# Kernel tuning notes

Hardware: AMD Instinct MI355X
Metric: run time of the kernel (lower is better)

## Reference

```python
import jax, jax.numpy as jnp
import numpy as np

B, S, D, H, DFF = 2, 2048, 1024, 16, 4096
HD = D // H
EPS = 1e-5


def setup_inputs() -> dict:
    key = jax.random.key(0)
    ks = jax.random.split(key, 8)
    s = lambda fan_in: 1.0 / np.sqrt(fan_in)
    return {
        "x": jax.random.normal(ks[0], (B, S, D), jnp.float32),
        "ln1_g": jnp.ones((D,), jnp.float32),
        "ln1_b": jnp.zeros((D,), jnp.float32),
        "Wq": jax.random.normal(ks[1], (D, D), jnp.float32) * s(D),
        "Wk": jax.random.normal(ks[2], (D, D), jnp.float32) * s(D),
        "Wv": jax.random.normal(ks[3], (D, D), jnp.float32) * s(D),
        "Wo": jax.random.normal(ks[4], (D, D), jnp.float32) * s(D),
        "bo": jnp.zeros((D,), jnp.float32),
        "ln2_g": jnp.ones((D,), jnp.float32),
        "ln2_b": jnp.zeros((D,), jnp.float32),
        "W1": jax.random.normal(ks[5], (D, DFF), jnp.float32) * s(D),
        "b1": jnp.zeros((DFF,), jnp.float32),
        "W2": jax.random.normal(ks[6], (DFF, D), jnp.float32) * s(DFF),
        "b2": jnp.zeros((D,), jnp.float32),
    }


def _layernorm(x, g, b):
    mu = jnp.mean(x, axis=-1, keepdims=True)
    var = jnp.var(x, axis=-1, keepdims=True)
    return (x - mu) * jax.lax.rsqrt(var + EPS) * g + b


def reference(x, ln1_g, ln1_b, Wq, Wk, Wv, Wo, bo, ln2_g, ln2_b, W1, b1, W2, b2):
    # --- pre-LN + causal multi-head attention + residual ---
    h = _layernorm(x, ln1_g, ln1_b)
    q = (h @ Wq).reshape(B, S, H, HD).transpose(0, 2, 1, 3)  # [B,H,S,hd]
    k = (h @ Wk).reshape(B, S, H, HD).transpose(0, 2, 1, 3)
    v = (h @ Wv).reshape(B, S, H, HD).transpose(0, 2, 1, 3)
    scores = jnp.einsum("bhqd,bhkd->bhqk", q, k) / jnp.sqrt(jnp.float32(HD))
    causal = jnp.triu(jnp.ones((S, S), bool), k=1)  # True above diagonal -> masked
    scores = jnp.where(causal, -jnp.inf, scores)
    attn = jax.nn.softmax(scores, axis=-1)  # dropout is identity at inference
    ctx = jnp.einsum("bhqk,bhkd->bhqd", attn, v)
    ctx = ctx.transpose(0, 2, 1, 3).reshape(B, S, D)
    x = x + ctx @ Wo + bo
    # --- pre-LN + MLP + residual ---
    h = _layernorm(x, ln2_g, ln2_b)
    h = jax.nn.gelu(h @ W1 + b1, approximate=False)  # torch nn.GELU default = exact
    x = x + h @ W2 + b2
    return x
```

## Files before the change

kernel.cpp:

```cpp
#include <hip/hip_runtime.h>
#include <hip/hip_bf16.h>
#include <math.h>

using bf16 = __hip_bfloat16;
typedef short bf16x8 __attribute__((ext_vector_type(8)));
typedef float f32x4 __attribute__((ext_vector_type(4)));

static constexpr int B = 2, S = 2048, D = 1024, H = 16, HD = 64, DFF = 4096;
static constexpr int NR = B * S;
static constexpr int DQ = 3072;
static constexpr float EPS = 1e-5f;

__device__ __forceinline__ bf16 f2b(float v) { return __float2bfloat16(v); }

typedef __attribute__((address_space(1))) const void* gp1_t;
typedef __attribute__((address_space(3))) void* sp3_t;
__device__ __forceinline__ void gld_lds16(const bf16* g, bf16* l) {
    __builtin_amdgcn_global_load_lds((gp1_t)(const void*)g, (sp3_t)(void*)l, 16, 0, 0);
}

__device__ __forceinline__ void convT_body(const float* __restrict__ src,
                                           bf16* __restrict__ dst,
                                           int K, int N, int k0, int n0, int tid) {
    __shared__ float tile[64][65];
    const int r = tid >> 4, c = (tid & 15) * 4;
#pragma unroll
    for (int rr = 0; rr < 64; rr += 16) {
        float4 v = *(const float4*)&src[(size_t)(k0 + r + rr) * N + n0 + c];
        tile[r + rr][c] = v.x; tile[r + rr][c + 1] = v.y;
        tile[r + rr][c + 2] = v.z; tile[r + rr][c + 3] = v.w;
    }
    __syncthreads();
    const int n = tid >> 2, ks = (tid & 3) * 16;
    union { bf16 h[16]; int4 v2[2]; } o;
#pragma unroll
    for (int i = 0; i < 16; ++i) o.h[i] = f2b(tile[ks + i][n]);
    bf16* dp = &dst[(size_t)(n0 + n) * K + k0 + ks];
    *(int4*)dp = o.v2[0];
    *(int4*)(dp + 8) = o.v2[1];
}

__global__ __launch_bounds__(256) void convT_kernel(const float* __restrict__ src,
                                                    bf16* __restrict__ dst,
                                                    int K, int N) {
    convT_body(src, dst, K, N, blockIdx.x * 64, blockIdx.y * 64, threadIdx.x);
}

__global__ __launch_bounds__(256) void convT5_kernel(const float* __restrict__ Wq,
                                                     const float* __restrict__ Wk,
                                                     const float* __restrict__ Wv,
                                                     const float* __restrict__ Wo,
                                                     const float* __restrict__ W2,
                                                     bf16* __restrict__ WqkvT,
                                                     bf16* __restrict__ WoT,
                                                     bf16* __restrict__ W2T) {
    const int bid = blockIdx.x;
    const float* src;
    bf16* dst;
    int K, N, bx, by;
    if (bid < 768) {
        const int j = bid >> 8, r = bid & 255;
        src = (j == 0) ? Wq : ((j == 1) ? Wk : Wv);
        dst = WqkvT + (size_t)j * D * D;
        K = D; N = D; bx = r & 15; by = r >> 4;
    } else if (bid < 1024) {
        const int r = bid - 768;
        src = Wo; dst = WoT; K = D; N = D; bx = r & 15; by = r >> 4;
    } else {
        const int r = bid - 1024;
        src = W2; dst = W2T; K = DFF; N = D; bx = r & 63; by = r >> 6;
    }
    convT_body(src, dst, K, N, bx * 64, by * 64, threadIdx.x);
}

__global__ __launch_bounds__(256) void ln_kernel(const float* __restrict__ x,
                                                 const float* __restrict__ g,
                                                 const float* __restrict__ b,
                                                 bf16* __restrict__ out) {
    const int row = blockIdx.x;
    const int tid = threadIdx.x;
    const float4 v4 = ((const float4*)(x + (size_t)row * D))[tid];
    float v[4] = {v4.x, v4.y, v4.z, v4.w};
    float s = v[0] + v[1] + v[2] + v[3];
    float sq = v[0] * v[0] + v[1] * v[1] + v[2] * v[2] + v[3] * v[3];
#pragma unroll
    for (int off = 32; off >= 1; off >>= 1) {
        s += __shfl_xor(s, off);
        sq += __shfl_xor(sq, off);
    }
    __shared__ float ssum[4], ssq[4];
    const int wave = tid >> 6;
    if ((tid & 63) == 0) { ssum[wave] = s; ssq[wave] = sq; }
    __syncthreads();
    s = ssum[0] + ssum[1] + ssum[2] + ssum[3];
    sq = ssq[0] + ssq[1] + ssq[2] + ssq[3];
    const float mu = s * (1.0f / D);
    const float var = sq * (1.0f / D) - mu * mu;
    const float rstd = rsqrtf(var + EPS);
    bf16* orow = out + (size_t)row * D;
#pragma unroll
    for (int i = 0; i < 4; ++i) {
        const int c = tid * 4 + i;
        orow[c] = f2b((v[i] - mu) * rstd * g[c] + b[c]);
    }
}

template <int EPI, int BN, int TPB>
__global__ __launch_bounds__(256) void gemm_bt(const bf16* __restrict__ A,
                                               const bf16* __restrict__ Bt,
                                               const float* __restrict__ bias,
                                               const float* __restrict__ res,
                                               void* __restrict__ Cv,
                                               int M, int N, int K) {
    constexpr int NTW = BN / 32;
    constexpr int AHALF = 128 * 32;
    constexpr int BHALF = BN * 32;
    constexpr int ASZ = 2 * AHALF, BSZ = 2 * BHALF;
    constexpr int CST = BN + 8;
    __shared__ __align__(16) bf16 smem[2 * (ASZ + BSZ)];

    const int Mtiles = M / 128;
    const int p = blockIdx.x;
    const int tm = p % Mtiles;
    const int tn0 = (p / Mtiles) * TPB;
    const int tid = threadIdx.x;
    const int wave = tid >> 6, lane = tid & 63;
    const int wm = wave >> 1, wn = wave & 1;
    const int quad = lane >> 4, l16 = lane & 15;

    const int r4 = tid >> 2, s4 = (tid & 3) * 8;
    const size_t K64 = (size_t)64 * K;
    const int nk = K / 64;

    for (int tp = 0; tp < TPB; ++tp) {
        const int tn = tn0 + tp;
        if (tp) __syncthreads();

        f32x4 acc[4][NTW];
#pragma unroll
        for (int i = 0; i < 4; ++i)
#pragma unroll
            for (int j = 0; j < NTW; ++j) acc[i][j] = (f32x4){0.f, 0.f, 0.f, 0.f};

        const bf16* Ap = A + (size_t)(tm * 128 + r4) * K + s4;
        const bf16* Bp = Bt + (size_t)(tn * BN + r4) * K + s4;

        gld_lds16(Ap, smem + tid * 8);
        gld_lds16(Ap + K64, smem + (256 + tid) * 8);
        gld_lds16(Ap + 32, smem + (512 + tid) * 8);
        gld_lds16(Ap + K64 + 32, smem + (768 + tid) * 8);
        gld_lds16(Bp, smem + 2 * ASZ + tid * 8);
        gld_lds16(Bp + 32, smem + 2 * ASZ + (256 + tid) * 8);
        Ap += 64;
        Bp += 64;

        for (int kt = 0; kt < nk; ++kt) {
            const int cur = kt & 1, nxt = cur ^ 1;
            bf16* Acur = smem + cur * ASZ;
            bf16* Bcur = smem + 2 * ASZ + cur * BSZ;
            __syncthreads();
            if (kt + 1 < nk) {
                bf16* Anxt = smem + nxt * ASZ;
                bf16* Bnxt = smem + 2 * ASZ + nxt * BSZ;
                gld_lds16(Ap, Anxt + tid * 8);
                gld_lds16(Ap + K64, Anxt + (256 + tid) * 8);
                gld_lds16(Ap + 32, Anxt + (512 + tid) * 8);
                gld_lds16(Ap + K64 + 32, Anxt + (768 + tid) * 8);
                gld_lds16(Bp, Bnxt + tid * 8);
                gld_lds16(Bp + 32, Bnxt + (256 + tid) * 8);
                Ap += 64;
                Bp += 64;
            }

#pragma unroll
            for (int ks = 0; ks < 2; ++ks) {
                const bf16* Ah = Acur + ks * AHALF;
                const bf16* Bh = Bcur + ks * BHALF;
                bf16x8 aF[4], bF[NTW];
#pragma unroll
                for (int mt = 0; mt < 4; ++mt)
                    aF[mt] = *(const bf16x8*)(Ah + (wm * 64 + mt * 16 + l16) * 32 + quad * 8);
#pragma unroll
                for (int nt = 0; nt < NTW; ++nt)
                    bF[nt] = *(const bf16x8*)(Bh + (wn * (BN / 2) + nt * 16 + l16) * 32 + quad * 8);
#pragma unroll
                for (int mt = 0; mt < 4; ++mt)
#pragma unroll
                    for (int nt = 0; nt < NTW; ++nt)
                        acc[mt][nt] = __builtin_amdgcn_mfma_f32_16x16x32_bf16(
                            aF[mt], bF[nt], acc[mt][nt], 0, 0, 0);
            }
        }

        if constexpr (EPI == 1) {
#pragma unroll
            for (int nt = 0; nt < NTW; ++nt) {
                const int col = tn * BN + wn * (BN / 2) + nt * 16 + l16;
                const float bv = bias[col];
#pragma unroll
                for (int mt = 0; mt < 4; ++mt) {
                    const int row0 = tm * 128 + wm * 64 + mt * 16 + quad * 4;
#pragma unroll
                    for (int j = 0; j < 4; ++j) {
                        const size_t idx = (size_t)(row0 + j) * N + col;
                        ((float*)Cv)[idx] = acc[mt][nt][j] + bv + res[idx];
                    }
                }
            }
        } else {
            bf16* C = (bf16*)Cv;
            __syncthreads();
#pragma unroll
            for (int nt = 0; nt < NTW; ++nt) {
                const int ccol = wn * (BN / 2) + nt * 16 + l16;
                float bv = 0.f;
                if (EPI == 2) bv = bias[tn * BN + ccol];
#pragma unroll
                for (int mt = 0; mt < 4; ++mt) {
                    const int r0 = wm * 64 + mt * 16 + quad * 4;
#pragma unroll
                    for (int j = 0; j < 4; ++j) {
                        float v = acc[mt][nt][j];
                        if (EPI == 2) {
                            v += bv;
                            v = 0.5f * v * (1.0f + erff(v * 0.70710678118654752f));
                        }
                        smem[(r0 + j) * CST + ccol] = f2b(v);
                    }
                }
            }
            __syncthreads();
            bf16* crow = C + (size_t)(tm * 128) * N + tn * BN;
#pragma unroll
            for (int i = 0; i < BN / 16; ++i) {
                const int gid = i * 256 + tid;
                const int row = gid / (BN / 8), c8 = gid % (BN / 8);
                const int4 val = *(const int4*)(smem + row * CST + c8 * 8);
                *(int4*)(crow + (size_t)row * N + c8 * 8) = val;
            }
        }
    }
}

__global__ __launch_bounds__(256) void fattn_kernel(const bf16* __restrict__ QKV,
                                                    bf16* __restrict__ ctx) {
    const int id = blockIdx.x;
    const int bh = id & 31;
    const int k = id >> 5;
    const int t = (k < 16) ? 31 - k : k - 16;
    const int b = bh >> 4, h = bh & (H - 1);
    const int tid = threadIdx.x;
    const int wave = tid >> 6, lane = tid & 63;
    const int quad = lane >> 4, l16 = lane & 15;
    const bf16* Qp = QKV + (size_t)b * S * DQ + h * HD;
    const bf16* Kp = Qp + D;
    const bf16* Vp = Qp + 2 * D;

    __shared__ __align__(16) bf16 Ks[2][64 * 64];
    __shared__ __align__(16) bf16 Vt[2][64][72];

    const int keyA = tid >> 3;
    const int sA = (keyA & 3) | ((keyA >> 1) & 4);
    const int dsA = ((tid & 7) ^ sA) * 8;
    const size_t K32 = (size_t)32 * DQ;

    const int q0 = t * 64;
    const bf16* qg = Qp + (size_t)(q0 + wave * 16 + l16) * DQ + quad * 8;
    union U8 { bf16 h[8]; bf16x8 v; };
    U8 uq0, uq1;
    uq0.v = *(const bf16x8*)(qg);
    uq1.v = *(const bf16x8*)(qg + 32);
#pragma unroll
    for (int i = 0; i < 8; ++i) {
        uq0.h[i] = f2b(__bfloat162float(uq0.h[i]) * 0.125f);
        uq1.h[i] = f2b(__bfloat162float(uq1.h[i]) * 0.125f);
    }
    const bf16x8 aQ0 = uq0.v;
    const bf16x8 aQ1 = uq1.v;

    const int kb = (l16 >> 2) * 8 + (l16 & 3);
    const int sQ = (l16 & 3) | (((l16 >> 2) & 1) << 2);
    const int ofs0 = kb * 64 + ((quad ^ sQ) * 8);
    const int ofs1 = kb * 64 + (((4 + quad) ^ sQ) * 8);

    f32x4 O[4];
#pragma unroll
    for (int nt = 0; nt < 4; ++nt) O[nt] = (f32x4){0.f, 0.f, 0.f, 0.f};
    float rowm = -3.0e38f, rowl = 0.f;

    gld_lds16(Kp + (size_t)keyA * DQ + dsA, Ks[0] + tid * 8);
    gld_lds16(Kp + K32 + (size_t)keyA * DQ + dsA, Ks[0] + (256 + tid) * 8);
    {
        const bf16* vg = Vp + (size_t)lane * DQ + wave * 16;
        U8 u0, u1;
        u0.v = *(const bf16x8*)vg;
        u1.v = *(const bf16x8*)(vg + 8);
#pragma unroll
        for (int i = 0; i < 8; ++i) {
            Vt[0][wave * 16 + i][lane] = u0.h[i];
            Vt[0][wave * 16 + 8 + i][lane] = u1.h[i];
        }
    }

    const int nch = t + 1;
    for (int c = 0; c < nch; ++c) {
        const int cur = c & 1, nxt = cur ^ 1;
        __syncthreads();
        U8 u0, u1;
        if (c + 1 < nch) {
            const bf16* kg = Kp + (size_t)((c + 1) * 64 + keyA) * DQ + dsA;
            gld_lds16(kg, Ks[nxt] + tid * 8);
            gld_lds16(kg + K32, Ks[nxt] + (256 + tid) * 8);
            const bf16* vg = Vp + (size_t)((c + 1) * 64 + lane) * DQ + wave * 16;
            u0.v = *(const bf16x8*)vg;
            u1.v = *(const bf16x8*)(vg + 8);
        }

        f32x4 sc[4];
        __builtin_amdgcn_s_setprio(1);
#pragma unroll
        for (int m = 0; m < 4; ++m) {
            const bf16* kr = Ks[cur] + (m & 1) * 256 + (m >> 1) * 2048;
            const bf16x8 bK0 = *(const bf16x8*)(kr + ofs0);
            const bf16x8 bK1 = *(const bf16x8*)(kr + ofs1);
            f32x4 z = (f32x4){0.f, 0.f, 0.f, 0.f};
            z = __builtin_amdgcn_mfma_f32_16x16x32_bf16(bK0, aQ0, z, 0, 0, 0);
            z = __builtin_amdgcn_mfma_f32_16x16x32_bf16(bK1, aQ1, z, 0, 0, 0);
            sc[m] = z;
        }
        __builtin_amdgcn_s_setprio(0);
        if (c == nch - 1) {
            const int qloc = wave * 16 + l16;
#pragma unroll
            for (int m = 0; m < 4; ++m) {
                const int kk = quad * 8 + (m & 1) * 4 + (m >> 1) * 32;
#pragma unroll
                for (int j = 0; j < 4; ++j)
                    if (kk + j > qloc) sc[m][j] = -3.0e38f;
            }
        }
        f32x4 mv;
#pragma unroll
        for (int j = 0; j < 4; ++j)
            mv[j] = fmaxf(fmaxf(sc[0][j], sc[1][j]), fmaxf(sc[2][j], sc[3][j]));
        float mx = fmaxf(fmaxf(mv[0], mv[1]), fmaxf(mv[2], mv[3]));
        mx = fmaxf(mx, __shfl_xor(mx, 16));
        mx = fmaxf(mx, __shfl_xor(mx, 32));
        const float mn = fmaxf(rowm, mx);
        const float alq = __expf(rowm - mn);
        rowm = mn;
        float rs = 0.f;
#pragma unroll
        for (int m = 0; m < 4; ++m)
#pragma unroll
            for (int j = 0; j < 4; ++j) {
                sc[m][j] = __expf(sc[m][j] - mn);
                rs += sc[m][j];
            }
        rs += __shfl_xor(rs, 16);
        rs += __shfl_xor(rs, 32);
        rowl = rowl * alq + rs;

        U8 p0, p1;
#pragma unroll
        for (int j = 0; j < 4; ++j) {
            p0.h[j]     = f2b(sc[0][j]);
            p0.h[4 + j] = f2b(sc[1][j]);
            p1.h[j]     = f2b(sc[2][j]);
            p1.h[4 + j] = f2b(sc[3][j]);
        }
#pragma unroll
        for (int nt = 0; nt < 4; ++nt)
#pragma unroll
            for (int j = 0; j < 4; ++j) O[nt][j] *= alq;
        __builtin_amdgcn_s_setprio(1);
#pragma unroll
        for (int nt = 0; nt < 4; ++nt) {
            const bf16x8 bV0 = *(const bf16x8*)&Vt[cur][nt * 16 + l16][quad * 8];
            const bf16x8 bV1 = *(const bf16x8*)&Vt[cur][nt * 16 + l16][32 + quad * 8];
            O[nt] = __builtin_amdgcn_mfma_f32_16x16x32_bf16(bV0, p0.v, O[nt], 0, 0, 0);
            O[nt] = __builtin_amdgcn_mfma_f32_16x16x32_bf16(bV1, p1.v, O[nt], 0, 0, 0);
        }
        __builtin_amdgcn_s_setprio(0);
        if (c + 1 < nch) {
#pragma unroll
            for (int i = 0; i < 8; ++i) {
                Vt[nxt][wave * 16 + i][lane] = u0.h[i];
                Vt[nxt][wave * 16 + 8 + i][lane] = u1.h[i];
            }
        }
    }

    const float rlq = 1.0f / rowl;
    bf16* crow = ctx + (size_t)b * S * D + h * HD + (size_t)(q0 + wave * 16 + l16) * D;
#pragma unroll
    for (int nt = 0; nt < 4; ++nt) {
        union { bf16 h[4]; int2 v; } o;
#pragma unroll
        for (int j = 0; j < 4; ++j) o.h[j] = f2b(O[nt][j] * rlq);
        *(int2*)(crow + nt * 16 + quad * 4) = o.v;
    }
}

extern "C" void kernel_launch(void* const* d_in, const int* in_sizes, int n_in,
                              void* d_out, int out_size, void* d_ws, size_t ws_size,
                              hipStream_t stream) {
    const float* x     = (const float*)d_in[0];
    const float* ln1_g = (const float*)d_in[1];
    const float* ln1_b = (const float*)d_in[2];
    const float* Wq    = (const float*)d_in[3];
    const float* Wk    = (const float*)d_in[4];
    const float* Wv    = (const float*)d_in[5];
    const float* Wo    = (const float*)d_in[6];
    const float* bo    = (const float*)d_in[7];
    const float* ln2_g = (const float*)d_in[8];
    const float* ln2_b = (const float*)d_in[9];
    const float* W1    = (const float*)d_in[10];
    const float* b1    = (const float*)d_in[11];
    const float* W2    = (const float*)d_in[12];
    const float* b2    = (const float*)d_in[13];
    float* out = (float*)d_out;

    char* ws = (char*)d_ws;
    const size_t MB = (size_t)1 << 20;
    bf16* h     = (bf16*)(ws + 0 * MB);
    bf16* W1T   = (bf16*)(ws + 0 * MB);
    bf16* QKVb  = (bf16*)(ws + 8 * MB);
    bf16* hff   = (bf16*)(ws + 8 * MB);
    bf16* ctx   = (bf16*)(ws + 32 * MB);
    bf16* h2    = (bf16*)(ws + 40 * MB);
    bf16* WqkvT = (bf16*)(ws + 48 * MB);
    bf16* WoT   = (bf16*)(ws + 54 * MB);
    bf16* W2T   = (bf16*)(ws + 56 * MB);

    convT5_kernel<<<2048, 256, 0, stream>>>(Wq, Wk, Wv, Wo, W2, WqkvT, WoT, W2T);
    ln_kernel<<<NR, 256, 0, stream>>>(x, ln1_g, ln1_b, h);
    gemm_bt<0, 64, 1><<<(NR / 128) * (DQ / 64), 256, 0, stream>>>(
        h, WqkvT, nullptr, nullptr, QKVb, NR, DQ, D);
    convT_kernel<<<dim3(16, 64), 256, 0, stream>>>(W1, W1T, D, DFF);
    fattn_kernel<<<dim3((S / 64) * B * H), 256, 0, stream>>>(QKVb, ctx);
    gemm_bt<1, 64, 1><<<(NR / 128) * (D / 64), 256, 0, stream>>>(
        ctx, WoT, bo, x, out, NR, D, D);
    ln_kernel<<<NR, 256, 0, stream>>>(out, ln2_g, ln2_b, h2);
    gemm_bt<2, 64, 1><<<(NR / 128) * (DFF / 64), 256, 0, stream>>>(
        h2, W1T, b1, nullptr, hff, NR, DFF, D);
    gemm_bt<1, 64, 1><<<(NR / 128) * (D / 64), 256, 0, stream>>>(
        hff, W2T, b2, out, out, NR, D, DFF);
}
```

Baseline: 334.4 us.

## Use polynomial erf GELU, lazy softmax rescaling, and fuse W1 transpose into batch conversion

Replaces the library erff in the MLP GELU epilogue with an Abramowitz-Stegun rational polynomial using a fast reciprocal and exp. In flash attention, the running max and output rescale are updated only when any lane's chunk max exceeds the current max by more than 8, skipping per-chunk O multiplies. When the workspace is large enough, the W1 transpose is folded into the batched weight-conversion kernel, removing a separate launch. Risks are a small loss of GELU accuracy and larger unnormalized exponentials in attention.

```diff
diff --git a/kernel.cpp b/kernel.cpp
--- a/kernel.cpp
+++ b/kernel.cpp
@@ -12,6 +12,20 @@
 static constexpr float EPS = 1e-5f;
 
 __device__ __forceinline__ bf16 f2b(float v) { return __float2bfloat16(v); }
+
+__device__ __forceinline__ float gelu_exact(float v) {
+    const float u = v * 0.70710678118654752f;
+    const float au = fabsf(u);
+    const float t = __builtin_amdgcn_rcpf(1.0f + 0.3275911f * au);
+    float poly = 1.061405429f;
+    poly = poly * t - 1.453152027f;
+    poly = poly * t + 1.421413741f;
+    poly = poly * t - 0.284496736f;
+    poly = poly * t + 0.254829592f;
+    poly = poly * t;
+    const float ea = 1.0f - poly * __expf(-u * u);
+    return 0.5f * v * (1.0f + copysignf(ea, u));
+}
 
 typedef __attribute__((address_space(1))) const void* gp1_t;
 typedef __attribute__((address_space(3))) void* sp3_t;
@@ -46,14 +60,16 @@
     convT_body(src, dst, K, N, blockIdx.x * 64, blockIdx.y * 64, threadIdx.x);
 }
 
-__global__ __launch_bounds__(256) void convT5_kernel(const float* __restrict__ Wq,
+__global__ __launch_bounds__(256) void convT6_kernel(const float* __restrict__ Wq,
                                                      const float* __restrict__ Wk,
                                                      const float* __restrict__ Wv,
                                                      const float* __restrict__ Wo,
                                                      const float* __restrict__ W2,
+                                                     const float* __restrict__ W1,
                                                      bf16* __restrict__ WqkvT,
                                                      bf16* __restrict__ WoT,
-                                                     bf16* __restrict__ W2T) {
+                                                     bf16* __restrict__ W2T,
+                                                     bf16* __restrict__ W1T) {
     const int bid = blockIdx.x;
     const float* src;
     bf16* dst;
@@ -66,9 +82,12 @@
     } else if (bid < 1024) {
         const int r = bid - 768;
         src = Wo; dst = WoT; K = D; N = D; bx = r & 15; by = r >> 4;
-    } else {
+    } else if (bid < 2048) {
         const int r = bid - 1024;
         src = W2; dst = W2T; K = DFF; N = D; bx = r & 63; by = r >> 6;
+    } else {
+        const int r = bid - 2048;
+        src = W1; dst = W1T; K = D; N = DFF; bx = r & 15; by = r >> 4;
     }
     convT_body(src, dst, K, N, bx * 64, by * 64, threadIdx.x);
 }
@@ -221,10 +240,7 @@
 #pragma unroll
                     for (int j = 0; j < 4; ++j) {
                         float v = acc[mt][nt][j];
-                        if (EPI == 2) {
-                            v += bv;
-                            v = 0.5f * v * (1.0f + erff(v * 0.70710678118654752f));
-                        }
+                        if (EPI == 2) v = gelu_exact(v + bv);
                         smem[(r0 + j) * CST + ccol] = f2b(v);
                     }
                 }
@@ -346,20 +362,27 @@
         float mx = fmaxf(fmaxf(mv[0], mv[1]), fmaxf(mv[2], mv[3]));
         mx = fmaxf(mx, __shfl_xor(mx, 16));
         mx = fmaxf(mx, __shfl_xor(mx, 32));
-        const float mn = fmaxf(rowm, mx);
-        const float alq = __expf(rowm - mn);
-        rowm = mn;
+        if (__any(mx > rowm + 8.0f)) {
+            const float mn = fmaxf(rowm, mx);
+            const float alq = __expf(rowm - mn);
+            rowm = mn;
+            rowl *= alq;
+#pragma unroll
+            for (int nt = 0; nt < 4; ++nt)
+#pragma unroll
+                for (int j = 0; j < 4; ++j) O[nt][j] *= alq;
+        }
         float rs = 0.f;
 #pragma unroll
         for (int m = 0; m < 4; ++m)
 #pragma unroll
             for (int j = 0; j < 4; ++j) {
-                sc[m][j] = __expf(sc[m][j] - mn);
+                sc[m][j] = __expf(sc[m][j] - rowm);
                 rs += sc[m][j];
             }
         rs += __shfl_xor(rs, 16);
         rs += __shfl_xor(rs, 32);
-        rowl = rowl * alq + rs;
+        rowl += rs;
 
         U8 p0, p1;
 #pragma unroll
@@ -369,10 +392,6 @@
             p1.h[j]     = f2b(sc[2][j]);
             p1.h[4 + j] = f2b(sc[3][j]);
         }
-#pragma unroll
-        for (int nt = 0; nt < 4; ++nt)
-#pragma unroll
-            for (int j = 0; j < 4; ++j) O[nt][j] *= alq;
         __builtin_amdgcn_s_setprio(1);
 #pragma unroll
         for (int nt = 0; nt < 4; ++nt) {
@@ -423,8 +442,8 @@
 
     char* ws = (char*)d_ws;
     const size_t MB = (size_t)1 << 20;
+    const bool wide = ws_size >= 72 * MB;
     bf16* h     = (bf16*)(ws + 0 * MB);
-    bf16* W1T   = (bf16*)(ws + 0 * MB);
     bf16* QKVb  = (bf16*)(ws + 8 * MB);
     bf16* hff   = (bf16*)(ws + 8 * MB);
     bf16* ctx   = (bf16*)(ws + 32 * MB);
@@ -432,12 +451,14 @@
     bf16* WqkvT = (bf16*)(ws + 48 * MB);
     bf16* WoT   = (bf16*)(ws + 54 * MB);
     bf16* W2T   = (bf16*)(ws + 56 * MB);
-
-    convT5_kernel<<<2048, 256, 0, stream>>>(Wq, Wk, Wv, Wo, W2, WqkvT, WoT, W2T);
+    bf16* W1T   = wide ? (bf16*)(ws + 64 * MB) : (bf16*)(ws + 0 * MB);
+
+    convT6_kernel<<<wide ? 3072 : 2048, 256, 0, stream>>>(
+        Wq, Wk, Wv, Wo, W2, W1, WqkvT, WoT, W2T, W1T);
     ln_kernel<<<NR, 256, 0, stream>>>(x, ln1_g, ln1_b, h);
     gemm_bt<0, 64, 1><<<(NR / 128) * (DQ / 64), 256, 0, stream>>>(
         h, WqkvT, nullptr, nullptr, QKVb, NR, DQ, D);
-    convT_kernel<<<dim3(16, 64), 256, 0, stream>>>(W1, W1T, D, DFF);
+    if (!wide) convT_kernel<<<dim3(16, 64), 256, 0, stream>>>(W1, W1T, D, DFF);
     fattn_kernel<<<dim3((S / 64) * B * H), 256, 0, stream>>>(QKVb, ctx);
     gemm_bt<1, 64, 1><<<(NR / 128) * (D / 64), 256, 0, stream>>>(
         ctx, WoT, bo, x, out, NR, D, D);
```

New measurement: 320.0 us. 4.3% less time.
